# Optimization experiments

Hardware: AMD Instinct MI355X
Metric: run time of the kernel (lower is better)

Reference implementation:

```python
import jax, jax.numpy as jnp
import numpy as np

K_TOP = 2          # hardcoded k in MyAttentionFunction
S = 32             # hardcoded spatial size (interpolate to 32x32)
N = S * S          # 1024 patches (patch_size=1, stride=1 unfold)
NEG = jnp.float32(-1e30)  # stand-in for excluding columns from top-k


def setup_inputs() -> dict:
    key = jax.random.key(0)
    k1, k2, k3 = jax.random.split(key, 3)
    C = 4096
    generated = jax.random.normal(k1, (1, C, S, S), dtype=jnp.float32)
    known = jax.random.normal(k2, (1, C, S, S), dtype=jnp.float32)
    mask = jax.random.randint(k3, (1, 1, S, S), 0, 2).astype(jnp.float32)
    return {"generated": generated, "known": known, "mask": mask}


def _forward(generated, known, mask):
    C = generated.shape[1]
    # F.interpolate(mask, (32,32)) nearest, then flatten -> flag in {0,1}, shape (N,)
    flag = jax.image.resize(mask, (1, 1, S, S), method="nearest").reshape(N)
    # MyUnfold(x, 1, 1) == [1, N, C]; drop batch dim of 1.
    P = generated.reshape(C, N).T   # (N, C) patches of `generated`
    Kp = known.reshape(C, N).T      # (N, C) patches of `known`

    norm_p = jnp.sum(P * P, axis=-1)   # (N,)
    norm_k = jnp.sum(Kp * Kp, axis=-1)
    # Full cosine matrices; original restricts rows to flag==1 and columns to
    # flag==0 (cosine0) / flag==1 (cosine1) by extraction; we mask columns with
    # a very negative value so top-k returns the same values with GLOBAL indices
    # (which is exactly what the original reconstructs via nonzero()[indexes]).
    cos0 = (P @ Kp.T) / jnp.sqrt(norm_p[:, None] * norm_k[None, :])  # (N, N)
    cos1 = (P @ P.T) / jnp.sqrt(norm_p[:, None] * norm_p[None, :])
    cos0 = jnp.where(flag[None, :] == 0, cos0, NEG)
    cos1 = jnp.where(flag[None, :] == 1, cos1, NEG)

    w0, i0 = jax.lax.top_k(cos0, K_TOP)  # (N, k) values / global indices
    w1, i1 = jax.lax.top_k(cos1, K_TOP)

    m = flag                      # 1.0 on masked rows
    nm = jnp.sum(m)               # number of masked patches
    # weight means taken only over masked rows, then softmax (original uses
    # .item() + numpy softmax, i.e. detached constants).
    means = jnp.stack(
        [jnp.sum(w0[:, i] * m) / nm for i in range(K_TOP)]
        + [jnp.sum(w1[:, i] * m) / nm for i in range(K_TOP)]
    )
    weights = jax.lax.stop_gradient(jax.nn.softmax(means))  # (2k,)

    # The original builds dense 1024x1024 indicator matrices and bmm's them;
    # each indicator row for a masked patch is one-hot at its retrieved source,
    # so the bmm is just a gather into masked rows. The advanced-indexing quirk
    # ind[mask_idx, src_idx] (nonzero() pairs include a leading 0 column) also
    # unconditionally sets ind[0,0]=1; we reproduce that (set semantics: no
    # double count if row 0 already maps to column 0).
    rtn = jnp.zeros((N, C), dtype=generated.dtype)
    for i in range(2 * K_TOP):
        src = Kp if i < K_TOP else P
        cols = (i0 if i < K_TOP else i1)[:, i % K_TOP]  # (N,) global indices
        out_i = jnp.where(m[:, None] == 1, src[cols], 0.0)  # masked rows only
        dup = 1.0 - ((m[0] == 1) & (cols[0] == 0)).astype(src.dtype)
        out_i = out_i.at[0].add(src[0] * dup)  # spurious ind[0,0]=1 artifact
        rtn = rtn + weights[i] * out_i

    rtn = rtn.reshape(1, S, S, C).transpose(0, 3, 1, 2)  # (1, C, 32, 32)
    return jnp.concatenate([generated, known, rtn], axis=1)


def reference(generated, known, mask):
    return _forward(generated, known, mask)
```

## Files before the change

kernel.cpp:

```cpp
#include <hip/hip_runtime.h>
#include <hip/hip_bf16.h>
#include <math.h>

#define N_TOT 1024
#define C_DIM 4096
#define T_MARGIN 3e-4f

typedef __attribute__((ext_vector_type(8))) _Float16 half8;
typedef __attribute__((ext_vector_type(8))) unsigned short ushort8;
typedef __attribute__((ext_vector_type(8))) char schar8;
typedef __attribute__((ext_vector_type(4))) float floatx4;

__device__ inline unsigned short f2h(float v) {
    _Float16 h = (_Float16)v;
    return __builtin_bit_cast(unsigned short, h);
}
__device__ inline float h2f(unsigned short u) {
    return (float)__builtin_bit_cast(_Float16, u);
}
__device__ inline char lo_enc(float v, unsigned short h) {
    int e = (h >> 10) & 31;
    float lo = v - h2f(h);
    float q = rintf(lo * 240.0f * __uint_as_float((unsigned)(152 - e) << 23));
    q = fmaxf(-127.0f, fminf(127.0f, q));
    return (char)(int)q;
}
__device__ inline float lo_dec(char q, unsigned short h) {
    int e = (h >> 10) & 31;
    return (float)q * __uint_as_float((unsigned)(e + 102) << 23) * (1.0f / 240.0f);
}

__device__ inline void ins2(float v, int s, float& v1, int& s1, float& v2, int& s2) {
    if (v > v1 || (v == v1 && s < s1)) { v2 = v1; s2 = s1; v1 = v; s1 = s; }
    else if (v > v2 || (v == v2 && s < s2)) { v2 = v; s2 = s; }
}

__global__ __launch_bounds__(256) void split_norms(const float* __restrict__ G,
                                                   const float* __restrict__ Kn,
                                                   const float* __restrict__ flag,
                                                   unsigned short* __restrict__ Phi,
                                                   char* __restrict__ Plo,
                                                   unsigned short* __restrict__ Khi,
                                                   char* __restrict__ Klo,
                                                   float* __restrict__ normP,
                                                   float* __restrict__ normK,
                                                   int* __restrict__ colidx,
                                                   int* __restrict__ n0p) {
    const int z = blockIdx.z;
    const float* X = z ? Kn : G;
    unsigned short* Xhi = z ? Khi : Phi;
    char* Xlo = z ? Klo : Plo;
    float* normX = z ? normK : normP;

    __shared__ float tile[64 * 65];
    const int t  = threadIdx.x;
    const int c0 = blockIdx.x * 64;
    const int n0 = blockIdx.y * 64;

    #pragma unroll
    for (int s = 0; s < 4; s++) {
        int c_loc = s * 16 + (t >> 4);
        int n4    = (t & 15) * 4;
        float4 v = *(const float4*)&X[(size_t)(c0 + c_loc) * N_TOT + n0 + n4];
        tile[c_loc * 65 + n4 + 0] = v.x;
        tile[c_loc * 65 + n4 + 1] = v.y;
        tile[c_loc * 65 + n4 + 2] = v.z;
        tile[c_loc * 65 + n4 + 3] = v.w;
    }
    __syncthreads();

    #pragma unroll
    for (int s = 0; s < 2; s++) {
        int n_loc = s * 32 + (t >> 3);
        float fl = flag[n0 + n_loc];
        bool need = z ? (fl == 0.0f) : (fl == 1.0f);
        if (need) {
            int c8 = (t & 7) * 8;
            unsigned short h[8]; char l[8];
            float s2 = 0.0f;
            #pragma unroll
            for (int e = 0; e < 8; e++) {
                float v = tile[(c8 + e) * 65 + n_loc];
                s2 = fmaf(v, v, s2);
                h[e] = f2h(v);
                l[e] = lo_enc(v, h[e]);
            }
            s2 += __shfl_xor(s2, 1);
            s2 += __shfl_xor(s2, 2);
            s2 += __shfl_xor(s2, 4);
            if ((t & 7) == 0) atomicAdd(&normX[n0 + n_loc], s2);

            size_t base = (size_t)(n0 + n_loc) * C_DIM + c0 + c8;
            ushort8 hv; schar8 lv;
            #pragma unroll
            for (int e = 0; e < 8; e++) { hv[e] = h[e]; lv[e] = l[e]; }
            *(ushort8*)&Xhi[base] = hv;
            *(schar8*)&Xlo[base]  = lv;
        }
    }

    if (blockIdx.x == 0 && blockIdx.y == 0 && blockIdx.z == 0) {
        __shared__ int cz[256];
        __shared__ int co[256];
        float4 fv = *(const float4*)&flag[4 * t];
        int f[4] = {fv.x == 0.0f, fv.y == 0.0f, fv.z == 0.0f, fv.w == 0.0f};
        int nz = f[0] + f[1] + f[2] + f[3];
        cz[t] = nz; co[t] = 4 - nz;
        __syncthreads();
        for (int off = 1; off < 256; off <<= 1) {
            int vz = (t >= off) ? cz[t - off] : 0;
            int vo = (t >= off) ? co[t - off] : 0;
            __syncthreads();
            cz[t] += vz; co[t] += vo;
            __syncthreads();
        }
        const int fn0 = cz[255];
        int zs = cz[t] - nz;
        int os = fn0 + co[t] - (4 - nz);
        #pragma unroll
        for (int e = 0; e < 4; e++) {
            int j = 4 * t + e;
            if (f[e]) colidx[zs++] = j;
            else      colidx[os++] = j;
        }
        if (t == 0) *n0p = fn0;
    }
}

__global__ __launch_bounds__(256, 4) void gemm_coarse(const unsigned short* __restrict__ Phi,
                                                      const unsigned short* __restrict__ Khi,
                                                      const int* __restrict__ colidx,
                                                      const int* __restrict__ n0p,
                                                      float* __restrict__ dotPart) {
    const int n0 = *n0p;
    const int n1 = N_TOT - n0;
    const int ib = blockIdx.x * 64;
    if (ib >= n1) return;

    __shared__ unsigned short sA[64 * 64];
    __shared__ unsigned short sB[128 * 64];

    const int t    = threadIdx.x;
    const int wave = t >> 6, lane = t & 63;
    const int wm   = wave >> 1, wn = wave & 1;
    const int quad = lane >> 4, lrow = lane & 15;
    const int jb = blockIdx.y * 128;
    const int bz = blockIdx.z;
    const int k_beg = bz * 512;

    const int srow = t >> 3;
    const int g    = (t & 7) ^ (srow & 7);

    const unsigned short* gA[2];
    #pragma unroll
    for (int q = 0; q < 2; q++) {
        int r = ib + q * 32 + srow;
        int rr = (r < n1) ? r : (n1 - 1);
        gA[q] = Phi + (size_t)colidx[n0 + rr] * C_DIM + g * 8;
    }
    const unsigned short* gB[4];
    #pragma unroll
    for (int q = 0; q < 4; q++) {
        int s = jb + q * 32 + srow;
        int row = colidx[s];
        const unsigned short* src = (s < n0) ? Khi : Phi;
        gB[q] = src + (size_t)row * C_DIM + g * 8;
    }

    floatx4 acc[2][4] = {};

    for (int k0 = k_beg; k0 < k_beg + 512; k0 += 64) {
        #pragma unroll
        for (int q = 0; q < 2; q++)
            __builtin_amdgcn_global_load_lds(
                (const __attribute__((address_space(1))) void*)(gA[q] + k0),
                (__attribute__((address_space(3))) void*)((char*)sA + q * 4096 + t * 16), 16, 0, 0);
        #pragma unroll
        for (int q = 0; q < 4; q++)
            __builtin_amdgcn_global_load_lds(
                (const __attribute__((address_space(1))) void*)(gB[q] + k0),
                (__attribute__((address_space(3))) void*)((char*)sB + q * 4096 + t * 16), 16, 0, 0);
        __syncthreads();

        #pragma unroll
        for (int kk = 0; kk < 2; kk++) {
            const int gk = kk * 4 + quad;
            half8 a[2], b[4];
            #pragma unroll
            for (int ti = 0; ti < 2; ti++) {
                int m = wm * 32 + ti * 16 + lrow;
                a[ti] = *(const half8*)&sA[m * 64 + ((gk ^ (m & 7)) << 3)];
            }
            #pragma unroll
            for (int tj = 0; tj < 4; tj++) {
                int n = wn * 64 + tj * 16 + lrow;
                b[tj] = *(const half8*)&sB[n * 64 + ((gk ^ (n & 7)) << 3)];
            }
            #pragma unroll
            for (int ti = 0; ti < 2; ti++)
                #pragma unroll
                for (int tj = 0; tj < 4; tj++)
                    acc[ti][tj] = __builtin_amdgcn_mfma_f32_16x16x32_f16(a[ti], b[tj], acc[ti][tj], 0, 0, 0);
        }
        __syncthreads();
    }

    float* outp = dotPart + ((size_t)bz << 20);
    #pragma unroll
    for (int tj = 0; tj < 4; tj++) {
        int j = jb + wn * 64 + tj * 16 + lrow;
        #pragma unroll
        for (int ti = 0; ti < 2; ti++) {
            #pragma unroll
            for (int reg = 0; reg < 4; reg++) {
                int i = ib + wm * 32 + ti * 16 + quad * 4 + reg;
                outp[i * N_TOT + j] = acc[ti][tj][reg];
            }
        }
    }
}

__global__ __launch_bounds__(256) void select_k(const float* __restrict__ dotPart,
                                                const float* __restrict__ normP,
                                                const float* __restrict__ normK,
                                                const int* __restrict__ colidx,
                                                const int* __restrict__ n0p,
                                                float* __restrict__ w01,
                                                int* __restrict__ i01,
                                                int* __restrict__ wl_hdr,
                                                int* __restrict__ wl_cand) {
    __shared__ float sr_v1[2][4], sr_v2[2][4];
    __shared__ int   sr_s1[2][4], sr_s2[2][4];
    __shared__ int   s_cnt[2];
    __shared__ int   s_cand[2][16];

    const int r = blockIdx.x;
    const int t = threadIdx.x;
    const int n0 = *n0p;
    const int n1 = N_TOT - n0;
    if (r >= n1) {
        if (t < 2) wl_hdr[2 * r + t] = 0;
        return;
    }
    const int row = colidx[n0 + r];
    const int wave = t >> 6, lane = t & 63;
    const float nr = normP[row];

    if (t < 2) s_cnt[t] = 0;

    const float* base = dotPart + (size_t)r * N_TOT + 4 * t;
    float4 p0 = *(const float4*)(base);
    float4 p1 = *(const float4*)(base + (1ull << 20));
    float4 p2 = *(const float4*)(base + (2ull << 20));
    float4 p3 = *(const float4*)(base + (3ull << 20));
    float4 p4 = *(const float4*)(base + (4ull << 20));
    float4 p5 = *(const float4*)(base + (5ull << 20));
    float4 p6 = *(const float4*)(base + (6ull << 20));
    float4 p7 = *(const float4*)(base + (7ull << 20));
    float4 dv;
    dv.x = ((p0.x + p1.x) + (p2.x + p3.x)) + ((p4.x + p5.x) + (p6.x + p7.x));
    dv.y = ((p0.y + p1.y) + (p2.y + p3.y)) + ((p4.y + p5.y) + (p6.y + p7.y));
    dv.z = ((p0.z + p1.z) + (p2.z + p3.z)) + ((p4.z + p5.z) + (p6.z + p7.z));
    dv.w = ((p0.w + p1.w) + (p2.w + p3.w)) + ((p4.w + p5.w) + (p6.w + p7.w));

    float cv[4];
    #pragma unroll
    for (int e = 0; e < 4; e++) {
        int s = 4 * t + e;
        int gj = colidx[s];
        float nb = (s < n0) ? normK[gj] : normP[gj];
        float d  = (e == 0) ? dv.x : (e == 1) ? dv.y : (e == 2) ? dv.z : dv.w;
        cv[e] = d * rsqrtf(nr * nb);
    }

    #pragma unroll
    for (int zz = 0; zz < 2; zz++) {
        float v1 = -INFINITY, v2 = -INFINITY;
        int   s1 = 0x7FFFFFFF, s2 = 0x7FFFFFFF;
        #pragma unroll
        for (int e = 0; e < 4; e++) {
            int s = 4 * t + e;
            bool inz = zz ? (s >= n0) : (s < n0);
            if (inz) ins2(cv[e], s, v1, s1, v2, s2);
        }
        #pragma unroll
        for (int off = 32; off > 0; off >>= 1) {
            float o1 = __shfl_xor(v1, off); int q1 = __shfl_xor(s1, off);
            float o2 = __shfl_xor(v2, off); int q2 = __shfl_xor(s2, off);
            ins2(o1, q1, v1, s1, v2, s2);
            ins2(o2, q2, v1, s1, v2, s2);
        }
        if (lane == 0) {
            sr_v1[zz][wave] = v1; sr_s1[zz][wave] = s1;
            sr_v2[zz][wave] = v2; sr_s2[zz][wave] = s2;
        }
    }
    __syncthreads();

    float m1z[2], m2z[2]; int b1z[2], b2z[2];
    #pragma unroll
    for (int zz = 0; zz < 2; zz++) {
        float m1 = -INFINITY, m2 = -INFINITY;
        int   b1 = 0x7FFFFFFF, b2 = 0x7FFFFFFF;
        #pragma unroll
        for (int w = 0; w < 4; w++) {
            ins2(sr_v1[zz][w], sr_s1[zz][w], m1, b1, m2, b2);
            ins2(sr_v2[zz][w], sr_s2[zz][w], m1, b1, m2, b2);
        }
        m1z[zz] = m1; m2z[zz] = m2; b1z[zz] = b1; b2z[zz] = b2;
        const float thr = m2 - T_MARGIN;
        #pragma unroll
        for (int e = 0; e < 4; e++) {
            int s = 4 * t + e;
            bool inz = zz ? (s >= n0) : (s < n0);
            if (inz && cv[e] > thr) {
                int idx = atomicAdd(&s_cnt[zz], 1);
                if (idx < 16) s_cand[zz][idx] = s;
            }
        }
    }
    __syncthreads();

    bool need[2]; int cntz[2];
    #pragma unroll
    for (int zz = 0; zz < 2; zz++) {
        const int cnt = min(s_cnt[zz], 16);
        cntz[zz] = cnt;
        const bool trusted = (s_cnt[zz] == 2) && (m1z[zz] - m2z[zz] > T_MARGIN);
        need[zz] = !trusted;
        if (t == 0) {
            wl_hdr[2 * r + zz] = trusted ? 0 : cnt;
            if (trusted) {
                int base2 = (zz * N_TOT + row) * 2;
                w01[base2]     = m1z[zz];
                w01[base2 + 1] = m2z[zz];
                i01[base2]     = colidx[b1z[zz]];
                i01[base2 + 1] = colidx[b2z[zz]];
            }
        }
    }
    __syncthreads();

    #pragma unroll
    for (int zz = 0; zz < 2; zz++)
        if (need[zz] && t < cntz[zz])
            wl_cand[(2 * r + zz) * 16 + t] = s_cand[zz][t];
}

__global__ __launch_bounds__(256) void refine2(const unsigned short* __restrict__ Phi,
                                               const char* __restrict__ Plo,
                                               const unsigned short* __restrict__ Khi,
                                               const char* __restrict__ Klo,
                                               const float* __restrict__ normP,
                                               const float* __restrict__ normK,
                                               const int* __restrict__ colidx,
                                               const int* __restrict__ n0p,
                                               const int* __restrict__ wl_hdr,
                                               const int* __restrict__ wl_cand,
                                               float* __restrict__ w01,
                                               int* __restrict__ i01) {
    __shared__ float sAf[C_DIM];
    __shared__ float s_rcv[16];
    __shared__ int   s_rcj[16];

    const int item = blockIdx.x;
    const int cnt  = wl_hdr[item];
    if (cnt == 0) return;

    const int n0 = *n0p;
    const int r  = item >> 1;
    const int zz = item & 1;
    const int row = colidx[n0 + r];
    const int t   = threadIdx.x;
    const int grp = t >> 5, l32 = t & 31;
    const float nr = normP[row];

    {
        const unsigned short* Ah = Phi + (size_t)row * C_DIM;
        const char*           Al = Plo + (size_t)row * C_DIM;
        #pragma unroll
        for (int s = 0; s < 2; s++) {
            int c = t * 16 + s * 8;
            ushort8 hb = *(const ushort8*)&Ah[c];
            schar8  lb = *(const schar8*)&Al[c];
            #pragma unroll
            for (int e = 0; e < 8; e++) sAf[c + e] = h2f(hb[e]) + lo_dec(lb[e], hb[e]);
        }
    }
    __syncthreads();

    #pragma unroll
    for (int p = 0; p < 2; p++) {
        if (p == 1 && cnt <= 8) break;
        const int q = grp + 8 * p;
        float acc = 0.0f;
        int gj = 0; float nb = 1.0f;
        if (q < cnt) {
            const int cs = wl_cand[item * 16 + q];
            gj = colidx[cs];
            nb = (cs < n0) ? normK[gj] : normP[gj];
            const unsigned short* bh_row = ((cs < n0) ? Khi : Phi) + (size_t)gj * C_DIM;
            const char*           bl_row = ((cs < n0) ? Klo : Plo) + (size_t)gj * C_DIM;
            #pragma unroll 4
            for (int it = 0; it < 16; it++) {
                int c = it * 256 + l32 * 8;
                ushort8 hb = *(const ushort8*)&bh_row[c];
                schar8  lb = *(const schar8*)&bl_row[c];
                #pragma unroll
                for (int e = 0; e < 8; e++)
                    acc = fmaf(sAf[c + e], h2f(hb[e]) + lo_dec(lb[e], hb[e]), acc);
            }
        }
        #pragma unroll
        for (int off = 16; off > 0; off >>= 1) acc += __shfl_xor(acc, off);
        if (l32 == 0 && q < cnt) {
            s_rcv[q] = acc * rsqrtf(nr * nb);
            s_rcj[q] = gj;
        }
    }
    __syncthreads();

    if (t == 0) {
        float v1 = -INFINITY, v2 = -INFINITY;
        int   j1 = 0x7FFFFFFF, j2 = 0x7FFFFFFF;
        for (int q = 0; q < cnt; q++) {
            float cvx = s_rcv[q];
            int   j   = s_rcj[q];
            if (cvx > v1 || (cvx == v1 && j < j1)) {
                v2 = v1; j2 = j1; v1 = cvx; j1 = j;
            } else if (cvx > v2 || (cvx == v2 && j < j2)) {
                v2 = cvx; j2 = j;
            }
        }
        if (j1 == 0x7FFFFFFF) j1 = 0;
        if (j2 == 0x7FFFFFFF) j2 = j1;
        int base = (zz * N_TOT + row) * 2;
        w01[base]     = v1;
        w01[base + 1] = v2;
        i01[base]     = j1;
        i01[base + 1] = j2;
    }
}

__global__ __launch_bounds__(256) void output_kernel(const float* __restrict__ G,
                                                     const float* __restrict__ Kn,
                                                     const float* __restrict__ flag,
                                                     const float* __restrict__ w01,
                                                     const int* __restrict__ i01,
                                                     float* __restrict__ out) {
    __shared__ float sG[4][N_TOT];
    __shared__ float sKn[4][N_TOT];
    __shared__ float red[5][4];
    __shared__ float swts[4];
    const int c0 = blockIdx.x * 4;
    const int t  = threadIdx.x;
    const int n4 = t * 4;
    const int wave = t >> 6, lane = t & 63;

    float4 fv = *(const float4*)&flag[n4];
    const float fa[4] = {fv.x, fv.y, fv.z, fv.w};
    float pm[5] = {};
    #pragma unroll
    for (int e = 0; e < 4; e++) {
        int n = n4 + e;
        if (fa[e] == 1.0f) {
            pm[0] += 1.0f;
            pm[1] += w01[n * 2 + 0];
            pm[2] += w01[n * 2 + 1];
            pm[3] += w01[2 * N_TOT + n * 2 + 0];
            pm[4] += w01[2 * N_TOT + n * 2 + 1];
        }
    }
    #pragma unroll
    for (int i = 0; i < 5; i++)
        #pragma unroll
        for (int off = 32; off > 0; off >>= 1)
            pm[i] += __shfl_xor(pm[i], off);
    if (lane == 0) {
        #pragma unroll
        for (int i = 0; i < 5; i++) red[i][wave] = pm[i];
    }

    #pragma unroll
    for (int ch = 0; ch < 4; ch++) {
        int c = c0 + ch;
        float4 gv = *(const float4*)&G[c * N_TOT + n4];
        float4 kv = *(const float4*)&Kn[c * N_TOT + n4];
        *(float4*)&sG[ch][n4]  = gv;
        *(float4*)&sKn[ch][n4] = kv;
        *(float4*)&out[c * N_TOT + n4] = gv;
        *(float4*)&out[C_DIM * N_TOT + c * N_TOT + n4] = kv;
    }
    __syncthreads();

    if (t == 0) {
        float tot[5];
        #pragma unroll
        for (int i = 0; i < 5; i++)
            tot[i] = red[i][0] + red[i][1] + red[i][2] + red[i][3];
        float inv = 1.0f / tot[0];
        float mv[4] = {tot[1] * inv, tot[2] * inv, tot[3] * inv, tot[4] * inv};
        float mx = fmaxf(fmaxf(mv[0], mv[1]), fmaxf(mv[2], mv[3]));
        float e[4], s = 0.0f;
        #pragma unroll
        for (int q = 0; q < 4; q++) { e[q] = expf(mv[q] - mx); s += e[q]; }
        #pragma unroll
        for (int q = 0; q < 4; q++) swts[q] = e[q] / s;
    }
    __syncthreads();
    const float w0 = swts[0], w1 = swts[1], w2 = swts[2], w3 = swts[3];

    float val[4][4];
    #pragma unroll
    for (int e = 0; e < 4; e++) {
        int n = n4 + e;
        float v[4] = {0.f, 0.f, 0.f, 0.f};
        if (fa[e] == 1.0f) {
            int2 i0 = *(const int2*)&i01[n * 2];
            int2 i1 = *(const int2*)&i01[2 * N_TOT + n * 2];
            #pragma unroll
            for (int ch = 0; ch < 4; ch++)
                v[ch] = w0 * sKn[ch][i0.x] + w1 * sKn[ch][i0.y]
                      + w2 * sG[ch][i1.x]  + w3 * sG[ch][i1.y];
        }
        if (n == 0) {
            bool m0 = (flag[0] == 1.0f);
            int2 i0 = m0 ? *(const int2*)&i01[0]         : make_int2(-1, -1);
            int2 i1 = m0 ? *(const int2*)&i01[2 * N_TOT] : make_int2(-1, -1);
            #pragma unroll
            for (int ch = 0; ch < 4; ch++) {
                if (!(m0 && i0.x == 0)) v[ch] += w0 * sKn[ch][0];
                if (!(m0 && i0.y == 0)) v[ch] += w1 * sKn[ch][0];
                if (!(m0 && i1.x == 0)) v[ch] += w2 * sG[ch][0];
                if (!(m0 && i1.y == 0)) v[ch] += w3 * sG[ch][0];
            }
        }
        #pragma unroll
        for (int ch = 0; ch < 4; ch++) val[ch][e] = v[ch];
    }
    #pragma unroll
    for (int ch = 0; ch < 4; ch++)
        *(float4*)&out[2 * C_DIM * N_TOT + (c0 + ch) * N_TOT + n4] =
            make_float4(val[ch][0], val[ch][1], val[ch][2], val[ch][3]);
}

extern "C" void kernel_launch(void* const* d_in, const int* in_sizes, int n_in,
                              void* d_out, int out_size, void* d_ws, size_t ws_size,
                              hipStream_t stream) {
    const float* G    = (const float*)d_in[0];
    const float* Kn   = (const float*)d_in[1];
    const float* flag = (const float*)d_in[2];
    float* out = (float*)d_out;

    char* p = (char*)d_ws;
    unsigned short* Phi = (unsigned short*)p;  p += (size_t)N_TOT * C_DIM * 2;
    unsigned short* Khi = (unsigned short*)p;  p += (size_t)N_TOT * C_DIM * 2;
    char* Plo = p;                             p += (size_t)N_TOT * C_DIM;
    char* Klo = p;                             p += (size_t)N_TOT * C_DIM;
    float* dotPart = (float*)p;                p += (size_t)8 * N_TOT * N_TOT * 4;
    float* normP   = (float*)p;                p += N_TOT * 4;
    float* normK   = (float*)p;                p += N_TOT * 4;
    float* w01     = (float*)p;                p += 4 * N_TOT * 4;
    int*   i01     = (int*)p;                  p += 4 * N_TOT * 4;
    int*   colidx  = (int*)p;                  p += N_TOT * 4;
    int*   n0p     = (int*)p;                  p += 16;
    int*   wl_hdr  = (int*)p;                  p += 2 * N_TOT * 4;
    int*   wl_cand = (int*)p;

    hipMemsetAsync(normP, 0, 2 * N_TOT * sizeof(float), stream);

    split_norms<<<dim3(64, 16, 2), 256, 0, stream>>>(G, Kn, flag, Phi, Plo, Khi, Klo,
                                                     normP, normK, colidx, n0p);
    gemm_coarse<<<dim3(16, 8, 8), 256, 0, stream>>>(Phi, Khi, colidx, n0p, dotPart);
    select_k<<<1024, 256, 0, stream>>>(dotPart, normP, normK, colidx, n0p,
                                       w01, i01, wl_hdr, wl_cand);
    refine2<<<2048, 256, 0, stream>>>(Phi, Plo, Khi, Klo, normP, normK, colidx, n0p,
                                      wl_hdr, wl_cand, w01, i01);
    output_kernel<<<1024, 256, 0, stream>>>(G, Kn, flag, w01, i01, out);
}
```

Measured before the change: 155.6 us.

## Fuse five kernels into one persistent kernel with grid-wide barriers

Merges split_norms, gemm_coarse, select_k, refine2 and output_kernel into a single persistent kernel of 1024 blocks. The stages are separated by a software global barrier built on an atomic counter that is zeroed by the existing memset. The aim is to remove kernel launch gaps and tail effects between the stages. In exchange, every stage is forced into a grid-stride loop at 4 blocks per CU, and the spin barrier costs something each time. The barrier also relies on all 1024 blocks being resident at once, or the kernel deadlocks.

Result: slower. 573.3 us (+268.5%).

```diff
diff --git a/kernel.cpp b/kernel.cpp
--- a/kernel.cpp
+++ b/kernel.cpp
@@ -1,10 +1,10 @@
 #include <hip/hip_runtime.h>
-#include <hip/hip_bf16.h>
 #include <math.h>
 
 #define N_TOT 1024
 #define C_DIM 4096
 #define T_MARGIN 3e-4f
+#define NBLK 1024
 
 typedef __attribute__((ext_vector_type(8))) _Float16 half8;
 typedef __attribute__((ext_vector_type(8))) unsigned short ushort8;
@@ -35,513 +35,507 @@
     else if (v > v2 || (v == v2 && s < s2)) { v2 = v; s2 = s; }
 }
 
-__global__ __launch_bounds__(256) void split_norms(const float* __restrict__ G,
-                                                   const float* __restrict__ Kn,
-                                                   const float* __restrict__ flag,
-                                                   unsigned short* __restrict__ Phi,
-                                                   char* __restrict__ Plo,
-                                                   unsigned short* __restrict__ Khi,
-                                                   char* __restrict__ Klo,
-                                                   float* __restrict__ normP,
-                                                   float* __restrict__ normK,
-                                                   int* __restrict__ colidx,
-                                                   int* __restrict__ n0p) {
-    const int z = blockIdx.z;
-    const float* X = z ? Kn : G;
-    unsigned short* Xhi = z ? Khi : Phi;
-    char* Xlo = z ? Klo : Plo;
-    float* normX = z ? normK : normP;
-
-    __shared__ float tile[64 * 65];
-    const int t  = threadIdx.x;
-    const int c0 = blockIdx.x * 64;
-    const int n0 = blockIdx.y * 64;
-
-    #pragma unroll
-    for (int s = 0; s < 4; s++) {
-        int c_loc = s * 16 + (t >> 4);
-        int n4    = (t & 15) * 4;
-        float4 v = *(const float4*)&X[(size_t)(c0 + c_loc) * N_TOT + n0 + n4];
-        tile[c_loc * 65 + n4 + 0] = v.x;
-        tile[c_loc * 65 + n4 + 1] = v.y;
-        tile[c_loc * 65 + n4 + 2] = v.z;
-        tile[c_loc * 65 + n4 + 3] = v.w;
+__device__ inline void gbar(int* ctr) {
+    __syncthreads();
+    if (threadIdx.x == 0) {
+        __threadfence();
+        atomicAdd(ctr, 1);
+        while (atomicAdd(ctr, 0) < NBLK) __builtin_amdgcn_s_sleep(8);
+        __threadfence();
     }
     __syncthreads();
-
-    #pragma unroll
-    for (int s = 0; s < 2; s++) {
-        int n_loc = s * 32 + (t >> 3);
-        float fl = flag[n0 + n_loc];
-        bool need = z ? (fl == 0.0f) : (fl == 1.0f);
-        if (need) {
-            int c8 = (t & 7) * 8;
-            unsigned short h[8]; char l[8];
-            float s2 = 0.0f;
-            #pragma unroll
-            for (int e = 0; e < 8; e++) {
-                float v = tile[(c8 + e) * 65 + n_loc];
-                s2 = fmaf(v, v, s2);
-                h[e] = f2h(v);
-                l[e] = lo_enc(v, h[e]);
-            }
-            s2 += __shfl_xor(s2, 1);
-            s2 += __shfl_xor(s2, 2);
-            s2 += __shfl_xor(s2, 4);
-            if ((t & 7) == 0) atomicAdd(&normX[n0 + n_loc], s2);
-
-            size_t base = (size_t)(n0 + n_loc) * C_DIM + c0 + c8;
-            ushort8 hv; schar8 lv;
-            #pragma unroll
-            for (int e = 0; e < 8; e++) { hv[e] = h[e]; lv[e] = l[e]; }
-            *(ushort8*)&Xhi[base] = hv;
-            *(schar8*)&Xlo[base]  = lv;
-        }
-    }
-
-    if (blockIdx.x == 0 && blockIdx.y == 0 && blockIdx.z == 0) {
-        __shared__ int cz[256];
-        __shared__ int co[256];
-        float4 fv = *(const float4*)&flag[4 * t];
-        int f[4] = {fv.x == 0.0f, fv.y == 0.0f, fv.z == 0.0f, fv.w == 0.0f};
-        int nz = f[0] + f[1] + f[2] + f[3];
-        cz[t] = nz; co[t] = 4 - nz;
-        __syncthreads();
-        for (int off = 1; off < 256; off <<= 1) {
-            int vz = (t >= off) ? cz[t - off] : 0;
-            int vo = (t >= off) ? co[t - off] : 0;
-            __syncthreads();
-            cz[t] += vz; co[t] += vo;
-            __syncthreads();
-        }
-        const int fn0 = cz[255];
-        int zs = cz[t] - nz;
-        int os = fn0 + co[t] - (4 - nz);
-        #pragma unroll
-        for (int e = 0; e < 4; e++) {
-            int j = 4 * t + e;
-            if (f[e]) colidx[zs++] = j;
-            else      colidx[os++] = j;
-        }
-        if (t == 0) *n0p = fn0;
-    }
-}
-
-__global__ __launch_bounds__(256, 4) void gemm_coarse(const unsigned short* __restrict__ Phi,
-                                                      const unsigned short* __restrict__ Khi,
-                                                      const int* __restrict__ colidx,
-                                                      const int* __restrict__ n0p,
-                                                      float* __restrict__ dotPart) {
-    const int n0 = *n0p;
-    const int n1 = N_TOT - n0;
-    const int ib = blockIdx.x * 64;
-    if (ib >= n1) return;
-
-    __shared__ unsigned short sA[64 * 64];
-    __shared__ unsigned short sB[128 * 64];
-
-    const int t    = threadIdx.x;
-    const int wave = t >> 6, lane = t & 63;
-    const int wm   = wave >> 1, wn = wave & 1;
-    const int quad = lane >> 4, lrow = lane & 15;
-    const int jb = blockIdx.y * 128;
-    const int bz = blockIdx.z;
-    const int k_beg = bz * 512;
-
-    const int srow = t >> 3;
-    const int g    = (t & 7) ^ (srow & 7);
-
-    const unsigned short* gA[2];
-    #pragma unroll
-    for (int q = 0; q < 2; q++) {
-        int r = ib + q * 32 + srow;
-        int rr = (r < n1) ? r : (n1 - 1);
-        gA[q] = Phi + (size_t)colidx[n0 + rr] * C_DIM + g * 8;
-    }
-    const unsigned short* gB[4];
-    #pragma unroll
-    for (int q = 0; q < 4; q++) {
-        int s = jb + q * 32 + srow;
-        int row = colidx[s];
-        const unsigned short* src = (s < n0) ? Khi : Phi;
-        gB[q] = src + (size_t)row * C_DIM + g * 8;
-    }
-
-    floatx4 acc[2][4] = {};
-
-    for (int k0 = k_beg; k0 < k_beg + 512; k0 += 64) {
-        #pragma unroll
-        for (int q = 0; q < 2; q++)
-            __builtin_amdgcn_global_load_lds(
-                (const __attribute__((address_space(1))) void*)(gA[q] + k0),
-                (__attribute__((address_space(3))) void*)((char*)sA + q * 4096 + t * 16), 16, 0, 0);
-        #pragma unroll
-        for (int q = 0; q < 4; q++)
-            __builtin_amdgcn_global_load_lds(
-                (const __attribute__((address_space(1))) void*)(gB[q] + k0),
-                (__attribute__((address_space(3))) void*)((char*)sB + q * 4096 + t * 16), 16, 0, 0);
-        __syncthreads();
-
-        #pragma unroll
-        for (int kk = 0; kk < 2; kk++) {
-            const int gk = kk * 4 + quad;
-            half8 a[2], b[4];
-            #pragma unroll
-            for (int ti = 0; ti < 2; ti++) {
-                int m = wm * 32 + ti * 16 + lrow;
-                a[ti] = *(const half8*)&sA[m * 64 + ((gk ^ (m & 7)) << 3)];
-            }
-            #pragma unroll
-            for (int tj = 0; tj < 4; tj++) {
-                int n = wn * 64 + tj * 16 + lrow;
-                b[tj] = *(const half8*)&sB[n * 64 + ((gk ^ (n & 7)) << 3)];
-            }
-            #pragma unroll
-            for (int ti = 0; ti < 2; ti++)
-                #pragma unroll
-                for (int tj = 0; tj < 4; tj++)
-                    acc[ti][tj] = __builtin_amdgcn_mfma_f32_16x16x32_f16(a[ti], b[tj], acc[ti][tj], 0, 0, 0);
-        }
-        __syncthreads();
-    }
-
-    float* outp = dotPart + ((size_t)bz << 20);
-    #pragma unroll
-    for (int tj = 0; tj < 4; tj++) {
-        int j = jb + wn * 64 + tj * 16 + lrow;
-        #pragma unroll
-        for (int ti = 0; ti < 2; ti++) {
-            #pragma unroll
-            for (int reg = 0; reg < 4; reg++) {
-                int i = ib + wm * 32 + ti * 16 + quad * 4 + reg;
-                outp[i * N_TOT + j] = acc[ti][tj][reg];
-            }
-        }
-    }
-}
-
-__global__ __launch_bounds__(256) void select_k(const float* __restrict__ dotPart,
-                                                const float* __restrict__ normP,
-                                                const float* __restrict__ normK,
-                                                const int* __restrict__ colidx,
-                                                const int* __restrict__ n0p,
-                                                float* __restrict__ w01,
-                                                int* __restrict__ i01,
-                                                int* __restrict__ wl_hdr,
-                                                int* __restrict__ wl_cand) {
+}
+
+__global__ __launch_bounds__(256, 4) void mega(const float* __restrict__ G,
+                                               const float* __restrict__ Kn,
+                                               const float* __restrict__ flag,
+                                               unsigned short* __restrict__ Phi,
+                                               char* __restrict__ Plo,
+                                               unsigned short* __restrict__ Khi,
+                                               char* __restrict__ Klo,
+                                               float* __restrict__ normP,
+                                               float* __restrict__ normK,
+                                               int* __restrict__ colidx,
+                                               int* __restrict__ n0p,
+                                               int* __restrict__ bar,
+                                               float* __restrict__ dotPart,
+                                               float* __restrict__ w01,
+                                               int* __restrict__ i01,
+                                               int* __restrict__ wl_hdr,
+                                               int* __restrict__ wl_cand,
+                                               float* __restrict__ out) {
+    __shared__ __align__(16) char smem[32896];
     __shared__ float sr_v1[2][4], sr_v2[2][4];
     __shared__ int   sr_s1[2][4], sr_s2[2][4];
     __shared__ int   s_cnt[2];
     __shared__ int   s_cand[2][16];
-
-    const int r = blockIdx.x;
-    const int t = threadIdx.x;
+    __shared__ float s_rcv[16];
+    __shared__ int   s_rcj[16];
+    __shared__ float red[5][4];
+    __shared__ float swts[4];
+
+    const int t    = threadIdx.x;
+    const int wave = t >> 6, lane = t & 63;
+
+    {
+        float* tile = (float*)smem;
+        for (int item = blockIdx.x; item < 2048; item += NBLK) {
+            const int z  = item >> 10;
+            const int rem = item & 1023;
+            const int c0 = (rem & 63) * 64;
+            const int nb = (rem >> 6) * 64;
+            const float* X = z ? Kn : G;
+            unsigned short* Xhi = z ? Khi : Phi;
+            char* Xlo = z ? Klo : Plo;
+            float* normX = z ? normK : normP;
+
+            #pragma unroll
+            for (int s = 0; s < 4; s++) {
+                int c_loc = s * 16 + (t >> 4);
+                int n4    = (t & 15) * 4;
+                float4 v = *(const float4*)&X[(size_t)(c0 + c_loc) * N_TOT + nb + n4];
+                tile[c_loc * 65 + n4 + 0] = v.x;
+                tile[c_loc * 65 + n4 + 1] = v.y;
+                tile[c_loc * 65 + n4 + 2] = v.z;
+                tile[c_loc * 65 + n4 + 3] = v.w;
+            }
+            __syncthreads();
+
+            #pragma unroll
+            for (int s = 0; s < 2; s++) {
+                int n_loc = s * 32 + (t >> 3);
+                float fl = flag[nb + n_loc];
+                bool need = z ? (fl == 0.0f) : (fl == 1.0f);
+                if (need) {
+                    int c8 = (t & 7) * 8;
+                    unsigned short h[8]; char l[8];
+                    float s2 = 0.0f;
+                    #pragma unroll
+                    for (int e = 0; e < 8; e++) {
+                        float v = tile[(c8 + e) * 65 + n_loc];
+                        s2 = fmaf(v, v, s2);
+                        h[e] = f2h(v);
+                        l[e] = lo_enc(v, h[e]);
+                    }
+                    s2 += __shfl_xor(s2, 1);
+                    s2 += __shfl_xor(s2, 2);
+                    s2 += __shfl_xor(s2, 4);
+                    if ((t & 7) == 0) atomicAdd(&normX[nb + n_loc], s2);
+
+                    size_t base = (size_t)(nb + n_loc) * C_DIM + c0 + c8;
+                    ushort8 hv; schar8 lv;
+                    #pragma unroll
+                    for (int e = 0; e < 8; e++) { hv[e] = h[e]; lv[e] = l[e]; }
+                    *(ushort8*)&Xhi[base] = hv;
+                    *(schar8*)&Xlo[base]  = lv;
+                }
+            }
+            __syncthreads();
+        }
+
+        if (blockIdx.x == 0) {
+            int* cz = (int*)(smem + 16640);
+            int* co = (int*)(smem + 17664);
+            float4 fv = *(const float4*)&flag[4 * t];
+            int f[4] = {fv.x == 0.0f, fv.y == 0.0f, fv.z == 0.0f, fv.w == 0.0f};
+            int nz = f[0] + f[1] + f[2] + f[3];
+            cz[t] = nz; co[t] = 4 - nz;
+            __syncthreads();
+            for (int off = 1; off < 256; off <<= 1) {
+                int vz = (t >= off) ? cz[t - off] : 0;
+                int vo = (t >= off) ? co[t - off] : 0;
+                __syncthreads();
+                cz[t] += vz; co[t] += vo;
+                __syncthreads();
+            }
+            const int fn0 = cz[255];
+            int zs = cz[t] - nz;
+            int os = fn0 + co[t] - (4 - nz);
+            #pragma unroll
+            for (int e = 0; e < 4; e++) {
+                int j = 4 * t + e;
+                if (f[e]) colidx[zs++] = j;
+                else      colidx[os++] = j;
+            }
+            if (t == 0) *n0p = fn0;
+        }
+    }
+    gbar(&bar[0]);
+
     const int n0 = *n0p;
     const int n1 = N_TOT - n0;
-    if (r >= n1) {
-        if (t < 2) wl_hdr[2 * r + t] = 0;
-        return;
+
+    {
+        unsigned short* sA = (unsigned short*)smem;
+        unsigned short* sB = (unsigned short*)(smem + 8192);
+        const int nib = (n1 + 63) >> 6;
+        const int total1 = nib * 64;
+        const int wm = wave >> 1, wn = wave & 1;
+        const int quad = lane >> 4, lrow = lane & 15;
+        const int srow = t >> 3;
+        const int g    = (t & 7) ^ (srow & 7);
+
+        for (int item = blockIdx.x; item < total1; item += NBLK) {
+            const int ib = (item >> 6) * 64;
+            const int jb = ((item >> 3) & 7) * 128;
+            const int bz = item & 7;
+            const int k_beg = bz * 512;
+
+            const unsigned short* gA[2];
+            #pragma unroll
+            for (int q = 0; q < 2; q++) {
+                int r = ib + q * 32 + srow;
+                int rr = (r < n1) ? r : (n1 - 1);
+                gA[q] = Phi + (size_t)colidx[n0 + rr] * C_DIM + g * 8;
+            }
+            const unsigned short* gB[4];
+            #pragma unroll
+            for (int q = 0; q < 4; q++) {
+                int s = jb + q * 32 + srow;
+                int row = colidx[s];
+                const unsigned short* src = (s < n0) ? Khi : Phi;
+                gB[q] = src + (size_t)row * C_DIM + g * 8;
+            }
+
+            floatx4 acc[2][4] = {};
+
+            for (int k0 = k_beg; k0 < k_beg + 512; k0 += 64) {
+                #pragma unroll
+                for (int q = 0; q < 2; q++)
+                    __builtin_amdgcn_global_load_lds(
+                        (const __attribute__((address_space(1))) void*)(gA[q] + k0),
+                        (__attribute__((address_space(3))) void*)((char*)sA + q * 4096 + t * 16), 16, 0, 0);
+                #pragma unroll
+                for (int q = 0; q < 4; q++)
+                    __builtin_amdgcn_global_load_lds(
+                        (const __attribute__((address_space(1))) void*)(gB[q] + k0),
+                        (__attribute__((address_space(3))) void*)((char*)sB + q * 4096 + t * 16), 16, 0, 0);
+                __syncthreads();
+
+                #pragma unroll
+                for (int kk = 0; kk < 2; kk++) {
+                    const int gk = kk * 4 + quad;
+                    half8 a[2], b[4];
+                    #pragma unroll
+                    for (int ti = 0; ti < 2; ti++) {
+                        int m = wm * 32 + ti * 16 + lrow;
+                        a[ti] = *(const half8*)&sA[m * 64 + ((gk ^ (m & 7)) << 3)];
+                    }
+                    #pragma unroll
+                    for (int tj = 0; tj < 4; tj++) {
+                        int n = wn * 64 + tj * 16 + lrow;
+                        b[tj] = *(const half8*)&sB[n * 64 + ((gk ^ (n & 7)) << 3)];
+                    }
+                    #pragma unroll
+                    for (int ti = 0; ti < 2; ti++)
+                        #pragma unroll
+                        for (int tj = 0; tj < 4; tj++)
+                            acc[ti][tj] = __builtin_amdgcn_mfma_f32_16x16x32_f16(a[ti], b[tj], acc[ti][tj], 0, 0, 0);
+                }
+                __syncthreads();
+            }
+
+            float* outp = dotPart + ((size_t)bz << 20);
+            #pragma unroll
+            for (int tj = 0; tj < 4; tj++) {
+                int j = jb + wn * 64 + tj * 16 + lrow;
+                #pragma unroll
+                for (int ti = 0; ti < 2; ti++) {
+                    #pragma unroll
+                    for (int reg = 0; reg < 4; reg++) {
+                        int i = ib + wm * 32 + ti * 16 + quad * 4 + reg;
+                        outp[i * N_TOT + j] = acc[ti][tj][reg];
+                    }
+                }
+            }
+        }
     }
-    const int row = colidx[n0 + r];
-    const int wave = t >> 6, lane = t & 63;
-    const float nr = normP[row];
-
-    if (t < 2) s_cnt[t] = 0;
-
-    const float* base = dotPart + (size_t)r * N_TOT + 4 * t;
-    float4 p0 = *(const float4*)(base);
-    float4 p1 = *(const float4*)(base + (1ull << 20));
-    float4 p2 = *(const float4*)(base + (2ull << 20));
-    float4 p3 = *(const float4*)(base + (3ull << 20));
-    float4 p4 = *(const float4*)(base + (4ull << 20));
-    float4 p5 = *(const float4*)(base + (5ull << 20));
-    float4 p6 = *(const float4*)(base + (6ull << 20));
-    float4 p7 = *(const float4*)(base + (7ull << 20));
-    float4 dv;
-    dv.x = ((p0.x + p1.x) + (p2.x + p3.x)) + ((p4.x + p5.x) + (p6.x + p7.x));
-    dv.y = ((p0.y + p1.y) + (p2.y + p3.y)) + ((p4.y + p5.y) + (p6.y + p7.y));
-    dv.z = ((p0.z + p1.z) + (p2.z + p3.z)) + ((p4.z + p5.z) + (p6.z + p7.z));
-    dv.w = ((p0.w + p1.w) + (p2.w + p3.w)) + ((p4.w + p5.w) + (p6.w + p7.w));
-
-    float cv[4];
-    #pragma unroll
-    for (int e = 0; e < 4; e++) {
-        int s = 4 * t + e;
-        int gj = colidx[s];
-        float nb = (s < n0) ? normK[gj] : normP[gj];
-        float d  = (e == 0) ? dv.x : (e == 1) ? dv.y : (e == 2) ? dv.z : dv.w;
-        cv[e] = d * rsqrtf(nr * nb);
+    gbar(&bar[1]);
+
+    {
+        const int r = blockIdx.x;
+        if (r >= n1) {
+            if (t < 2) wl_hdr[2 * r + t] = 0;
+        } else {
+            const int row = colidx[n0 + r];
+            const float nr = normP[row];
+            if (t < 2) s_cnt[t] = 0;
+
+            const float* base = dotPart + (size_t)r * N_TOT + 4 * t;
+            float4 p0 = *(const float4*)(base);
+            float4 p1 = *(const float4*)(base + (1ull << 20));
+            float4 p2 = *(const float4*)(base + (2ull << 20));
+            float4 p3 = *(const float4*)(base + (3ull << 20));
+            float4 p4 = *(const float4*)(base + (4ull << 20));
+            float4 p5 = *(const float4*)(base + (5ull << 20));
+            float4 p6 = *(const float4*)(base + (6ull << 20));
+            float4 p7 = *(const float4*)(base + (7ull << 20));
+            float4 dv;
+            dv.x = ((p0.x + p1.x) + (p2.x + p3.x)) + ((p4.x + p5.x) + (p6.x + p7.x));
+            dv.y = ((p0.y + p1.y) + (p2.y + p3.y)) + ((p4.y + p5.y) + (p6.y + p7.y));
+            dv.z = ((p0.z + p1.z) + (p2.z + p3.z)) + ((p4.z + p5.z) + (p6.z + p7.z));
+            dv.w = ((p0.w + p1.w) + (p2.w + p3.w)) + ((p4.w + p5.w) + (p6.w + p7.w));
+
+            float cv[4];
+            #pragma unroll
+            for (int e = 0; e < 4; e++) {
+                int s = 4 * t + e;
+                int gj = colidx[s];
+                float nb = (s < n0) ? normK[gj] : normP[gj];
+                float d  = (e == 0) ? dv.x : (e == 1) ? dv.y : (e == 2) ? dv.z : dv.w;
+                cv[e] = d * rsqrtf(nr * nb);
+            }
+
+            #pragma unroll
+            for (int zz = 0; zz < 2; zz++) {
+                float v1 = -INFINITY, v2 = -INFINITY;
+                int   s1 = 0x7FFFFFFF, s2 = 0x7FFFFFFF;
+                #pragma unroll
+                for (int e = 0; e < 4; e++) {
+                    int s = 4 * t + e;
+                    bool inz = zz ? (s >= n0) : (s < n0);
+                    if (inz) ins2(cv[e], s, v1, s1, v2, s2);
+                }
+                #pragma unroll
+                for (int off = 32; off > 0; off >>= 1) {
+                    float o1 = __shfl_xor(v1, off); int q1 = __shfl_xor(s1, off);
+                    float o2 = __shfl_xor(v2, off); int q2 = __shfl_xor(s2, off);
+                    ins2(o1, q1, v1, s1, v2, s2);
+                    ins2(o2, q2, v1, s1, v2, s2);
+                }
+                if (lane == 0) {
+                    sr_v1[zz][wave] = v1; sr_s1[zz][wave] = s1;
+                    sr_v2[zz][wave] = v2; sr_s2[zz][wave] = s2;
+                }
+            }
+            __syncthreads();
+
+            float m1z[2], m2z[2]; int b1z[2], b2z[2];
+            #pragma unroll
+            for (int zz = 0; zz < 2; zz++) {
+                float m1 = -INFINITY, m2 = -INFINITY;
+                int   b1 = 0x7FFFFFFF, b2 = 0x7FFFFFFF;
+                #pragma unroll
+                for (int w = 0; w < 4; w++) {
+                    ins2(sr_v1[zz][w], sr_s1[zz][w], m1, b1, m2, b2);
+                    ins2(sr_v2[zz][w], sr_s2[zz][w], m1, b1, m2, b2);
+                }
+                m1z[zz] = m1; m2z[zz] = m2; b1z[zz] = b1; b2z[zz] = b2;
+                const float thr = m2 - T_MARGIN;
+                #pragma unroll
+                for (int e = 0; e < 4; e++) {
+                    int s = 4 * t + e;
+                    bool inz = zz ? (s >= n0) : (s < n0);
+                    if (inz && cv[e] > thr) {
+                        int idx = atomicAdd(&s_cnt[zz], 1);
+                        if (idx < 16) s_cand[zz][idx] = s;
+                    }
+                }
+            }
+            __syncthreads();
+
+            bool need[2]; int cntz[2];
+            #pragma unroll
+            for (int zz = 0; zz < 2; zz++) {
+                const int cnt = min(s_cnt[zz], 16);
+                cntz[zz] = cnt;
+                const bool trusted = (s_cnt[zz] == 2) && (m1z[zz] - m2z[zz] > T_MARGIN);
+                need[zz] = !trusted;
+                if (t == 0) {
+                    wl_hdr[2 * r + zz] = trusted ? 0 : cnt;
+                    if (trusted) {
+                        int base2 = (zz * N_TOT + row) * 2;
+                        w01[base2]     = m1z[zz];
+                        w01[base2 + 1] = m2z[zz];
+                        i01[base2]     = colidx[b1z[zz]];
+                        i01[base2 + 1] = colidx[b2z[zz]];
+                    }
+                }
+            }
+            __syncthreads();
+
+            #pragma unroll
+            for (int zz = 0; zz < 2; zz++)
+                if (need[zz] && t < cntz[zz])
+                    wl_cand[(2 * r + zz) * 16 + t] = s_cand[zz][t];
+        }
     }
-
-    #pragma unroll
-    for (int zz = 0; zz < 2; zz++) {
-        float v1 = -INFINITY, v2 = -INFINITY;
-        int   s1 = 0x7FFFFFFF, s2 = 0x7FFFFFFF;
+    gbar(&bar[2]);
+
+    {
+        float* sAf = (float*)smem;
+        const int grp = t >> 5, l32 = t & 31;
+        for (int item = blockIdx.x; item < 2048; item += NBLK) {
+            const int cnt = wl_hdr[item];
+            if (cnt != 0) {
+                const int r  = item >> 1;
+                const int zz = item & 1;
+                const int row = colidx[n0 + r];
+                const float nr = normP[row];
+
+                {
+                    const unsigned short* Ah = Phi + (size_t)row * C_DIM;
+                    const char*           Al = Plo + (size_t)row * C_DIM;
+                    #pragma unroll
+                    for (int s = 0; s < 2; s++) {
+                        int c = t * 16 + s * 8;
+                        ushort8 hb = *(const ushort8*)&Ah[c];
+                        schar8  lb = *(const schar8*)&Al[c];
+                        #pragma unroll
+                        for (int e = 0; e < 8; e++) sAf[c + e] = h2f(hb[e]) + lo_dec(lb[e], hb[e]);
+                    }
+                }
+                __syncthreads();
+
+                #pragma unroll
+                for (int p = 0; p < 2; p++) {
+                    if (p == 1 && cnt <= 8) break;
+                    const int q = grp + 8 * p;
+                    float acc = 0.0f;
+                    int gj = 0; float nb = 1.0f;
+                    if (q < cnt) {
+                        const int cs = wl_cand[item * 16 + q];
+                        gj = colidx[cs];
+                        nb = (cs < n0) ? normK[gj] : normP[gj];
+                        const unsigned short* bh_row = ((cs < n0) ? Khi : Phi) + (size_t)gj * C_DIM;
+                        const char*           bl_row = ((cs < n0) ? Klo : Plo) + (size_t)gj * C_DIM;
+                        #pragma unroll 4
+                        for (int it = 0; it < 16; it++) {
+                            int c = it * 256 + l32 * 8;
+                            ushort8 hb = *(const ushort8*)&bh_row[c];
+                            schar8  lb = *(const schar8*)&bl_row[c];
+                            #pragma unroll
+                            for (int e = 0; e < 8; e++)
+                                acc = fmaf(sAf[c + e], h2f(hb[e]) + lo_dec(lb[e], hb[e]), acc);
+                        }
+                    }
+                    #pragma unroll
+                    for (int off = 16; off > 0; off >>= 1) acc += __shfl_xor(acc, off);
+                    if (l32 == 0 && q < cnt) {
+                        s_rcv[q] = acc * rsqrtf(nr * nb);
+                        s_rcj[q] = gj;
+                    }
+                }
+                __syncthreads();
+
+                if (t == 0) {
+                    float v1 = -INFINITY, v2 = -INFINITY;
+                    int   j1 = 0x7FFFFFFF, j2 = 0x7FFFFFFF;
+                    for (int q = 0; q < cnt; q++) {
+                        float cvx = s_rcv[q];
+                        int   j   = s_rcj[q];
+                        if (cvx > v1 || (cvx == v1 && j < j1)) {
+                            v2 = v1; j2 = j1; v1 = cvx; j1 = j;
+                        } else if (cvx > v2 || (cvx == v2 && j < j2)) {
+                            v2 = cvx; j2 = j;
+                        }
+                    }
+                    if (j1 == 0x7FFFFFFF) j1 = 0;
+                    if (j2 == 0x7FFFFFFF) j2 = j1;
+                    int base = (zz * N_TOT + row) * 2;
+                    w01[base]     = v1;
+                    w01[base + 1] = v2;
+                    i01[base]     = j1;
+                    i01[base + 1] = j2;
+                }
+                __syncthreads();
+            }
+        }
+    }
+    gbar(&bar[3]);
+
+    {
+        float* sG  = (float*)smem;
+        float* sKn = (float*)(smem + 16384);
+        const int c0 = blockIdx.x * 4;
+        const int n4 = t * 4;
+
+        float4 fv = *(const float4*)&flag[n4];
+        const float fa[4] = {fv.x, fv.y, fv.z, fv.w};
+        float pm[5] = {};
         #pragma unroll
         for (int e = 0; e < 4; e++) {
-            int s = 4 * t + e;
-            bool inz = zz ? (s >= n0) : (s < n0);
-            if (inz) ins2(cv[e], s, v1, s1, v2, s2);
+            int n = n4 + e;
+            if (fa[e] == 1.0f) {
+                pm[0] += 1.0f;
+                pm[1] += w01[n * 2 + 0];
+                pm[2] += w01[n * 2 + 1];
+                pm[3] += w01[2 * N_TOT + n * 2 + 0];
+                pm[4] += w01[2 * N_TOT + n * 2 + 1];
+            }
         }
         #pragma unroll
-        for (int off = 32; off > 0; off >>= 1) {
-            float o1 = __shfl_xor(v1, off); int q1 = __shfl_xor(s1, off);
-            float o2 = __shfl_xor(v2, off); int q2 = __shfl_xor(s2, off);
-            ins2(o1, q1, v1, s1, v2, s2);
-            ins2(o2, q2, v1, s1, v2, s2);
-        }
+        for (int i = 0; i < 5; i++)
+            #pragma unroll
+            for (int off = 32; off > 0; off >>= 1)
+                pm[i] += __shfl_xor(pm[i], off);
         if (lane == 0) {
-            sr_v1[zz][wave] = v1; sr_s1[zz][wave] = s1;
-            sr_v2[zz][wave] = v2; sr_s2[zz][wave] = s2;
-        }
-    }
-    __syncthreads();
-
-    float m1z[2], m2z[2]; int b1z[2], b2z[2];
-    #pragma unroll
-    for (int zz = 0; zz < 2; zz++) {
-        float m1 = -INFINITY, m2 = -INFINITY;
-        int   b1 = 0x7FFFFFFF, b2 = 0x7FFFFFFF;
+            #pragma unroll
+            for (int i = 0; i < 5; i++) red[i][wave] = pm[i];
+        }
+
         #pragma unroll
-        for (int w = 0; w < 4; w++) {
-            ins2(sr_v1[zz][w], sr_s1[zz][w], m1, b1, m2, b2);
-            ins2(sr_v2[zz][w], sr_s2[zz][w], m1, b1, m2, b2);
-        }
-        m1z[zz] = m1; m2z[zz] = m2; b1z[zz] = b1; b2z[zz] = b2;
-        const float thr = m2 - T_MARGIN;
+        for (int ch = 0; ch < 4; ch++) {
+            int c = c0 + ch;
+            float4 gv = *(const float4*)&G[c * N_TOT + n4];
+            float4 kv = *(const float4*)&Kn[c * N_TOT + n4];
+            *(float4*)&sG[ch * N_TOT + n4]  = gv;
+            *(float4*)&sKn[ch * N_TOT + n4] = kv;
+            *(float4*)&out[c * N_TOT + n4] = gv;
+            *(float4*)&out[C_DIM * N_TOT + c * N_TOT + n4] = kv;
+        }
+        __syncthreads();
+
+        if (t == 0) {
+            float tot[5];
+            #pragma unroll
+            for (int i = 0; i < 5; i++)
+                tot[i] = red[i][0] + red[i][1] + red[i][2] + red[i][3];
+            float inv = 1.0f / tot[0];
+            float mv[4] = {tot[1] * inv, tot[2] * inv, tot[3] * inv, tot[4] * inv};
+            float mx = fmaxf(fmaxf(mv[0], mv[1]), fmaxf(mv[2], mv[3]));
+            float e[4], s = 0.0f;
+            #pragma unroll
+            for (int q = 0; q < 4; q++) { e[q] = expf(mv[q] - mx); s += e[q]; }
+            #pragma unroll
+            for (int q = 0; q < 4; q++) swts[q] = e[q] / s;
+        }
+        __syncthreads();
+        const float w0 = swts[0], w1 = swts[1], w2 = swts[2], w3 = swts[3];
+
+        float val[4][4];
         #pragma unroll
         for (int e = 0; e < 4; e++) {
-            int s = 4 * t + e;
-            bool inz = zz ? (s >= n0) : (s < n0);
-            if (inz && cv[e] > thr) {
-                int idx = atomicAdd(&s_cnt[zz], 1);
-                if (idx < 16) s_cand[zz][idx] = s;
-            }
-        }
+            int n = n4 + e;
+            float v[4] = {0.f, 0.f, 0.f, 0.f};
+            if (fa[e] == 1.0f) {
+                int2 i0 = *(const int2*)&i01[n * 2];
+                int2 i1 = *(const int2*)&i01[2 * N_TOT + n * 2];
+                #pragma unroll
+                for (int ch = 0; ch < 4; ch++)
+                    v[ch] = w0 * sKn[ch * N_TOT + i0.x] + w1 * sKn[ch * N_TOT + i0.y]
+                          + w2 * sG[ch * N_TOT + i1.x]  + w3 * sG[ch * N_TOT + i1.y];
+            }
+            if (n == 0) {
+                bool m0 = (flag[0] == 1.0f);
+                int2 i0 = m0 ? *(const int2*)&i01[0]         : make_int2(-1, -1);
+                int2 i1 = m0 ? *(const int2*)&i01[2 * N_TOT] : make_int2(-1, -1);
+                #pragma unroll
+                for (int ch = 0; ch < 4; ch++) {
+                    if (!(m0 && i0.x == 0)) v[ch] += w0 * sKn[ch * N_TOT];
+                    if (!(m0 && i0.y == 0)) v[ch] += w1 * sKn[ch * N_TOT];
+                    if (!(m0 && i1.x == 0)) v[ch] += w2 * sG[ch * N_TOT];
+                    if (!(m0 && i1.y == 0)) v[ch] += w3 * sG[ch * N_TOT];
+                }
+            }
+            #pragma unroll
+            for (int ch = 0; ch < 4; ch++) val[ch][e] = v[ch];
+        }
+        #pragma unroll
+        for (int ch = 0; ch < 4; ch++)
+            *(float4*)&out[2 * C_DIM * N_TOT + (c0 + ch) * N_TOT + n4] =
+                make_float4(val[ch][0], val[ch][1], val[ch][2], val[ch][3]);
     }
-    __syncthreads();
-
-    bool need[2]; int cntz[2];
-    #pragma unroll
-    for (int zz = 0; zz < 2; zz++) {
-        const int cnt = min(s_cnt[zz], 16);
-        cntz[zz] = cnt;
-        const bool trusted = (s_cnt[zz] == 2) && (m1z[zz] - m2z[zz] > T_MARGIN);
-        need[zz] = !trusted;
-        if (t == 0) {
-            wl_hdr[2 * r + zz] = trusted ? 0 : cnt;
-            if (trusted) {
-                int base2 = (zz * N_TOT + row) * 2;
-                w01[base2]     = m1z[zz];
-                w01[base2 + 1] = m2z[zz];
-                i01[base2]     = colidx[b1z[zz]];
-                i01[base2 + 1] = colidx[b2z[zz]];
-            }
-        }
-    }
-    __syncthreads();
-
-    #pragma unroll
-    for (int zz = 0; zz < 2; zz++)
-        if (need[zz] && t < cntz[zz])
-            wl_cand[(2 * r + zz) * 16 + t] = s_cand[zz][t];
-}
-
-__global__ __launch_bounds__(256) void refine2(const unsigned short* __restrict__ Phi,
-                                               const char* __restrict__ Plo,
-                                               const unsigned short* __restrict__ Khi,
-                                               const char* __restrict__ Klo,
-                                               const float* __restrict__ normP,
-                                               const float* __restrict__ normK,
-                                               const int* __restrict__ colidx,
-                                               const int* __restrict__ n0p,
-                                               const int* __restrict__ wl_hdr,
-                                               const int* __restrict__ wl_cand,
-                                               float* __restrict__ w01,
-                                               int* __restrict__ i01) {
-    __shared__ float sAf[C_DIM];
-    __shared__ float s_rcv[16];
-    __shared__ int   s_rcj[16];
-
-    const int item = blockIdx.x;
-    const int cnt  = wl_hdr[item];
-    if (cnt == 0) return;
-
-    const int n0 = *n0p;
-    const int r  = item >> 1;
-    const int zz = item & 1;
-    const int row = colidx[n0 + r];
-    const int t   = threadIdx.x;
-    const int grp = t >> 5, l32 = t & 31;
-    const float nr = normP[row];
-
-    {
-        const unsigned short* Ah = Phi + (size_t)row * C_DIM;
-        const char*           Al = Plo + (size_t)row * C_DIM;
-        #pragma unroll
-        for (int s = 0; s < 2; s++) {
-            int c = t * 16 + s * 8;
-            ushort8 hb = *(const ushort8*)&Ah[c];
-            schar8  lb = *(const schar8*)&Al[c];
-            #pragma unroll
-            for (int e = 0; e < 8; e++) sAf[c + e] = h2f(hb[e]) + lo_dec(lb[e], hb[e]);
-        }
-    }
-    __syncthreads();
-
-    #pragma unroll
-    for (int p = 0; p < 2; p++) {
-        if (p == 1 && cnt <= 8) break;
-        const int q = grp + 8 * p;
-        float acc = 0.0f;
-        int gj = 0; float nb = 1.0f;
-        if (q < cnt) {
-            const int cs = wl_cand[item * 16 + q];
-            gj = colidx[cs];
-            nb = (cs < n0) ? normK[gj] : normP[gj];
-            const unsigned short* bh_row = ((cs < n0) ? Khi : Phi) + (size_t)gj * C_DIM;
-            const char*           bl_row = ((cs < n0) ? Klo : Plo) + (size_t)gj * C_DIM;
-            #pragma unroll 4
-            for (int it = 0; it < 16; it++) {
-                int c = it * 256 + l32 * 8;
-                ushort8 hb = *(const ushort8*)&bh_row[c];
-                schar8  lb = *(const schar8*)&bl_row[c];
-                #pragma unroll
-                for (int e = 0; e < 8; e++)
-                    acc = fmaf(sAf[c + e], h2f(hb[e]) + lo_dec(lb[e], hb[e]), acc);
-            }
-        }
-        #pragma unroll
-        for (int off = 16; off > 0; off >>= 1) acc += __shfl_xor(acc, off);
-        if (l32 == 0 && q < cnt) {
-            s_rcv[q] = acc * rsqrtf(nr * nb);
-            s_rcj[q] = gj;
-        }
-    }
-    __syncthreads();
-
-    if (t == 0) {
-        float v1 = -INFINITY, v2 = -INFINITY;
-        int   j1 = 0x7FFFFFFF, j2 = 0x7FFFFFFF;
-        for (int q = 0; q < cnt; q++) {
-            float cvx = s_rcv[q];
-            int   j   = s_rcj[q];
-            if (cvx > v1 || (cvx == v1 && j < j1)) {
-                v2 = v1; j2 = j1; v1 = cvx; j1 = j;
-            } else if (cvx > v2 || (cvx == v2 && j < j2)) {
-                v2 = cvx; j2 = j;
-            }
-        }
-        if (j1 == 0x7FFFFFFF) j1 = 0;
-        if (j2 == 0x7FFFFFFF) j2 = j1;
-        int base = (zz * N_TOT + row) * 2;
-        w01[base]     = v1;
-        w01[base + 1] = v2;
-        i01[base]     = j1;
-        i01[base + 1] = j2;
-    }
-}
-
-__global__ __launch_bounds__(256) void output_kernel(const float* __restrict__ G,
-                                                     const float* __restrict__ Kn,
-                                                     const float* __restrict__ flag,
-                                                     const float* __restrict__ w01,
-                                                     const int* __restrict__ i01,
-                                                     float* __restrict__ out) {
-    __shared__ float sG[4][N_TOT];
-    __shared__ float sKn[4][N_TOT];
-    __shared__ float red[5][4];
-    __shared__ float swts[4];
-    const int c0 = blockIdx.x * 4;
-    const int t  = threadIdx.x;
-    const int n4 = t * 4;
-    const int wave = t >> 6, lane = t & 63;
-
-    float4 fv = *(const float4*)&flag[n4];
-    const float fa[4] = {fv.x, fv.y, fv.z, fv.w};
-    float pm[5] = {};
-    #pragma unroll
-    for (int e = 0; e < 4; e++) {
-        int n = n4 + e;
-        if (fa[e] == 1.0f) {
-            pm[0] += 1.0f;
-            pm[1] += w01[n * 2 + 0];
-            pm[2] += w01[n * 2 + 1];
-            pm[3] += w01[2 * N_TOT + n * 2 + 0];
-            pm[4] += w01[2 * N_TOT + n * 2 + 1];
-        }
-    }
-    #pragma unroll
-    for (int i = 0; i < 5; i++)
-        #pragma unroll
-        for (int off = 32; off > 0; off >>= 1)
-            pm[i] += __shfl_xor(pm[i], off);
-    if (lane == 0) {
-        #pragma unroll
-        for (int i = 0; i < 5; i++) red[i][wave] = pm[i];
-    }
-
-    #pragma unroll
-    for (int ch = 0; ch < 4; ch++) {
-        int c = c0 + ch;
-        float4 gv = *(const float4*)&G[c * N_TOT + n4];
-        float4 kv = *(const float4*)&Kn[c * N_TOT + n4];
-        *(float4*)&sG[ch][n4]  = gv;
-        *(float4*)&sKn[ch][n4] = kv;
-        *(float4*)&out[c * N_TOT + n4] = gv;
-        *(float4*)&out[C_DIM * N_TOT + c * N_TOT + n4] = kv;
-    }
-    __syncthreads();
-
-    if (t == 0) {
-        float tot[5];
-        #pragma unroll
-        for (int i = 0; i < 5; i++)
-            tot[i] = red[i][0] + red[i][1] + red[i][2] + red[i][3];
-        float inv = 1.0f / tot[0];
-        float mv[4] = {tot[1] * inv, tot[2] * inv, tot[3] * inv, tot[4] * inv};
-        float mx = fmaxf(fmaxf(mv[0], mv[1]), fmaxf(mv[2], mv[3]));
-        float e[4], s = 0.0f;
-        #pragma unroll
-        for (int q = 0; q < 4; q++) { e[q] = expf(mv[q] - mx); s += e[q]; }
-        #pragma unroll
-        for (int q = 0; q < 4; q++) swts[q] = e[q] / s;
-    }
-    __syncthreads();
-    const float w0 = swts[0], w1 = swts[1], w2 = swts[2], w3 = swts[3];
-
-    float val[4][4];
-    #pragma unroll
-    for (int e = 0; e < 4; e++) {
-        int n = n4 + e;
-        float v[4] = {0.f, 0.f, 0.f, 0.f};
-        if (fa[e] == 1.0f) {
-            int2 i0 = *(const int2*)&i01[n * 2];
-            int2 i1 = *(const int2*)&i01[2 * N_TOT + n * 2];
-            #pragma unroll
-            for (int ch = 0; ch < 4; ch++)
-                v[ch] = w0 * sKn[ch][i0.x] + w1 * sKn[ch][i0.y]
-                      + w2 * sG[ch][i1.x]  + w3 * sG[ch][i1.y];
-        }
-        if (n == 0) {
-            bool m0 = (flag[0] == 1.0f);
-            int2 i0 = m0 ? *(const int2*)&i01[0]         : make_int2(-1, -1);
-            int2 i1 = m0 ? *(const int2*)&i01[2 * N_TOT] : make_int2(-1, -1);
-            #pragma unroll
-            for (int ch = 0; ch < 4; ch++) {
-                if (!(m0 && i0.x == 0)) v[ch] += w0 * sKn[ch][0];
-                if (!(m0 && i0.y == 0)) v[ch] += w1 * sKn[ch][0];
-                if (!(m0 && i1.x == 0)) v[ch] += w2 * sG[ch][0];
-                if (!(m0 && i1.y == 0)) v[ch] += w3 * sG[ch][0];
-            }
-        }
-        #pragma unroll
-        for (int ch = 0; ch < 4; ch++) val[ch][e] = v[ch];
-    }
-    #pragma unroll
-    for (int ch = 0; ch < 4; ch++)
-        *(float4*)&out[2 * C_DIM * N_TOT + (c0 + ch) * N_TOT + n4] =
-            make_float4(val[ch][0], val[ch][1], val[ch][2], val[ch][3]);
 }
 
 extern "C" void kernel_launch(void* const* d_in, const int* in_sizes, int n_in,
@@ -560,6 +554,7 @@
     float* dotPart = (float*)p;                p += (size_t)8 * N_TOT * N_TOT * 4;
     float* normP   = (float*)p;                p += N_TOT * 4;
     float* normK   = (float*)p;                p += N_TOT * 4;
+    int*   bar     = (int*)p;                  p += 64;
     float* w01     = (float*)p;                p += 4 * N_TOT * 4;
     int*   i01     = (int*)p;                  p += 4 * N_TOT * 4;
     int*   colidx  = (int*)p;                  p += N_TOT * 4;
@@ -567,14 +562,9 @@
     int*   wl_hdr  = (int*)p;                  p += 2 * N_TOT * 4;
     int*   wl_cand = (int*)p;
 
-    hipMemsetAsync(normP, 0, 2 * N_TOT * sizeof(float), stream);
-
-    split_norms<<<dim3(64, 16, 2), 256, 0, stream>>>(G, Kn, flag, Phi, Plo, Khi, Klo,
-                                                     normP, normK, colidx, n0p);
-    gemm_coarse<<<dim3(16, 8, 8), 256, 0, stream>>>(Phi, Khi, colidx, n0p, dotPart);
-    select_k<<<1024, 256, 0, stream>>>(dotPart, normP, normK, colidx, n0p,
-                                       w01, i01, wl_hdr, wl_cand);
-    refine2<<<2048, 256, 0, stream>>>(Phi, Plo, Khi, Klo, normP, normK, colidx, n0p,
-                                      wl_hdr, wl_cand, w01, i01);
-    output_kernel<<<1024, 256, 0, stream>>>(G, Kn, flag, w01, i01, out);
-}
+    hipMemsetAsync(normP, 0, 2 * N_TOT * sizeof(float) + 64, stream);
+
+    mega<<<dim3(NBLK), dim3(256), 0, stream>>>(G, Kn, flag, Phi, Plo, Khi, Klo,
+                                               normP, normK, colidx, n0p, bar,
+                                               dotPart, w01, i01, wl_hdr, wl_cand, out);
+}
```
